# Kernel optimization log

Measured on AMD Instinct MI355X. Metric: run time of the kernel, lower is better.

Reference implementation:

```python
import jax, jax.numpy as jnp
import numpy as np

D_EQUI, D_INV, D_MSG, N_HEADS, D_FF = 64, 256, 64, 8, 256
D_EDGE_IN, D_EDGE_OUT = 64, 64
D_OUT = D_EQUI + N_HEADS + D_EDGE_OUT  # 136
IN_FEATS = 2 * D_MSG + D_EQUI + D_EDGE_IN  # 256
B, N = 4, 256
NEG_INF = -1e9  # finite stand-in for -inf in adj_to_attn_mask


def setup_inputs() -> dict:
    key = jax.random.key(0)
    ks = jax.random.split(key, 20)
    def rn(k, shape, scale):
        return jax.random.normal(k, shape, dtype=jnp.float32) * scale
    inp = {
        "equis": rn(ks[0], (B, N, 3, D_EQUI), 1.0),
        "invs": rn(ks[1], (B, N, D_INV), 1.0),
        "edges": rn(ks[2], (B, N, N, D_EDGE_IN), 1.0),
        "adj_matrix": jax.random.randint(ks[3], (B, N, N), 0, 2, dtype=jnp.int32),
        # _PairwiseMessages params
        "Wq": rn(ks[4], (D_MSG, D_INV), D_INV ** -0.5),
        "bq": jnp.zeros((D_MSG,), jnp.float32),
        "Wk": rn(ks[5], (D_MSG, D_INV), D_INV ** -0.5),
        "bk": jnp.zeros((D_MSG,), jnp.float32),
        "W1": rn(ks[6], (D_FF, IN_FEATS), IN_FEATS ** -0.5),
        "b1": jnp.zeros((D_FF,), jnp.float32),
        "W2": rn(ks[7], (D_OUT, D_FF), D_FF ** -0.5),
        "b2": jnp.zeros((D_OUT,), jnp.float32),
        # _EquiAttention params (no bias)
        "Wc": rn(ks[8], (D_EQUI, D_EQUI), D_EQUI ** -0.5),
        "Wa": rn(ks[9], (D_EQUI, D_EQUI), D_EQUI ** -0.5),
        # _InvAttention params
        "Wi": rn(ks[10], (D_INV, D_INV), D_INV ** -0.5),
        "bi": jnp.zeros((D_INV,), jnp.float32),
        "Wo": rn(ks[11], (D_INV, D_INV), D_INV ** -0.5),
        "bo": jnp.zeros((D_INV,), jnp.float32),
    }
    return inp


def _forward(equis, invs, edges, adj_matrix, Wq, bq, Wk, bk, W1, b1, W2, b2, Wc, Wa, Wi, bi, Wo, bo):
    # ---- _PairwiseMessages ----
    # per-channel dot products over the 3 coordinates: [B, Nq, Nk, d_equi]
    dotprods = jnp.einsum("bqcd,bkcd->bqkd", equis, equis)
    q_msg = invs @ Wq.T + bq          # [B, N, d_msg]
    k_msg = invs @ Wk.T + bk          # [B, N, d_msg]
    Nq = invs.shape[1]
    pairwise = jnp.concatenate(
        (
            jnp.broadcast_to(q_msg[:, :, None, :], (B, Nq, Nq, D_MSG)),
            jnp.broadcast_to(k_msg[:, None, :, :], (B, Nq, Nq, D_MSG)),
            dotprods,
            edges,
        ),
        axis=-1,
    )  # [B, Nq, Nk, in_feats]
    h = jax.nn.silu(pairwise @ W1.T + b1)
    messages = h @ W2.T + b2          # [B, Nq, Nk, d_out]

    equi_msg = messages[..., :D_EQUI]
    inv_msg = messages[..., D_EQUI : D_EQUI + N_HEADS]
    edge_out = messages[..., D_EQUI + N_HEADS :]

    attn_mask = jnp.where(adj_matrix > 0, 0.0, NEG_INF).astype(equi_msg.dtype)  # [B,Nq,Nk]

    # ---- _EquiAttention ----
    attn_e = jax.nn.softmax(equi_msg + attn_mask[..., None], axis=2)  # [B,Nq,Nk,d_equi]
    proj_equi = equis @ Wc.T                                          # [B,Nk,3,d_equi]
    attn_out_e = jnp.einsum("bqkd,bkcd->bqcd", attn_e, proj_equi)     # [B,Nq,3,d_equi]
    w_e = jnp.sqrt(jnp.sum(attn_e ** 2, axis=2))                      # [B,Nq,d_equi]
    attn_out_e = attn_out_e * w_e[:, :, None, :]
    equi_updates = attn_out_e @ Wa.T

    # ---- _InvAttention ----
    attn_i = jax.nn.softmax(inv_msg + attn_mask[..., None], axis=2)   # [B,Nq,Nk,H]
    proj_feats = invs @ Wi.T + bi                                     # [B,Nk,d_inv]
    head_feats = proj_feats.reshape(B, Nq, N_HEADS, D_INV // N_HEADS)
    attn_out_i = jnp.einsum("bqkh,bkhd->bqhd", attn_i, head_feats)    # [B,Nq,H,d_head]
    w_i = jnp.sqrt(jnp.sum(attn_i ** 2, axis=2))                      # [B,Nq,H]
    attn_out_i = attn_out_i * w_i[..., None]
    inv_updates = attn_out_i.reshape(B, Nq, D_INV) @ Wo.T + bo

    return equi_updates, inv_updates, edge_out


def reference(equis, invs, edges, adj_matrix, Wq, bq, Wk, bk, W1, b1, W2, b2, Wc, Wa, Wi, bi, Wo, bo):
    return _forward(equis, invs, edges, adj_matrix, Wq, bq, Wk, bk, W1, b1, W2, b2, Wc, Wa, Wi, bi, Wo, bo)
```

## Files before the change

kernel.cpp:

```cpp
#include <hip/hip_runtime.h>
#include <hip/hip_bf16.h>
#include <cstdint>


typedef __bf16 bf16x8_t __attribute__((ext_vector_type(8)));
typedef float  f32x4_t  __attribute__((ext_vector_type(4)));

#define SP 76
#define KV 32

__device__ __forceinline__ int swzX(int row, int col) {
    return row * 192 + (col ^ ((row & 7) << 3));
}
__device__ __forceinline__ int swzH(int row, int col) {
    return (row << 8) + (col ^ ((row & 7) << 3));
}

__device__ __forceinline__ bf16x8_t cvt8(f32x4_t a, f32x4_t b) {
    bf16x8_t r;
    r[0] = (__bf16)a.x; r[1] = (__bf16)a.y; r[2] = (__bf16)a.z; r[3] = (__bf16)a.w;
    r[4] = (__bf16)b.x; r[5] = (__bf16)b.y; r[6] = (__bf16)b.z; r[7] = (__bf16)b.w;
    return r;
}

__device__ __forceinline__ void lds_barrier() {
    asm volatile("s_waitcnt lgkmcnt(0)" ::: "memory");
    __builtin_amdgcn_s_barrier();
    asm volatile("" ::: "memory");
}

__global__ __launch_bounds__(256) void semla_pre(
    const float* __restrict__ invs, const float* __restrict__ equis,
    const float* __restrict__ Wq, const float* __restrict__ bq,
    const float* __restrict__ Wk, const float* __restrict__ bk,
    const float* __restrict__ Wc, const float* __restrict__ Wi, const float* __restrict__ bi,
    const float* __restrict__ W1, const float* __restrict__ W2,
    __bf16* __restrict__ W1bf, __bf16* __restrict__ W2bf,
    float* __restrict__ qc, float* __restrict__ kmsg,
    float* __restrict__ pTE, float* __restrict__ pTF)
{
    const int blk = blockIdx.x, tid = threadIdx.x;
    if (blk < 256) {
        const int r0 = blk * 4;
        __shared__ __align__(16) float sInv4[4][256];
        __shared__ __align__(16) float sEqu4[4][192];
        __shared__ __align__(16) float sQm4[4][64];
        #pragma unroll
        for (int j = 0; j < 4; ++j) {
            sInv4[j][tid] = invs[(size_t)(r0 + j) * 256 + tid];
            if (tid < 192) sEqu4[j][tid] = equis[(size_t)(r0 + j) * 192 + tid];
        }
        __syncthreads();
        {
            float acc[4] = {0.f, 0.f, 0.f, 0.f};
            const float* w = &Wi[tid * 256];
            for (int i = 0; i < 256; i += 4) {
                f32x4_t ww = *(const f32x4_t*)&w[i];
                #pragma unroll
                for (int j = 0; j < 4; ++j) {
                    const float* x = &sInv4[j][i];
                    acc[j] += ww.x * x[0] + ww.y * x[1] + ww.z * x[2] + ww.w * x[3];
                }
            }
            const float bb = bi[tid];
            #pragma unroll
            for (int j = 0; j < 4; ++j) {
                const int bb_ = (r0 + j) >> 8, nl = (r0 + j) & 255;
                pTF[((size_t)bb_ * 256 + tid) * 256 + nl] = acc[j] + bb;
            }
        }
        if (tid < 128) {
            const int d = tid & 63;
            const float* w = (tid < 64) ? &Wq[d * 256] : &Wk[d * 256];
            float acc[4] = {0.f, 0.f, 0.f, 0.f};
            for (int i = 0; i < 256; i += 4) {
                f32x4_t ww = *(const f32x4_t*)&w[i];
                #pragma unroll
                for (int j = 0; j < 4; ++j) {
                    const float* x = &sInv4[j][i];
                    acc[j] += ww.x * x[0] + ww.y * x[1] + ww.z * x[2] + ww.w * x[3];
                }
            }
            if (tid < 64) {
                const float bb = bq[d];
                #pragma unroll
                for (int j = 0; j < 4; ++j) sQm4[j][d] = acc[j] + bb;
            } else {
                const float bb = bk[d];
                #pragma unroll
                for (int j = 0; j < 4; ++j) kmsg[(size_t)(r0 + j) * 64 + d] = acc[j] + bb;
            }
        }
        if (tid < 192) {
            const int c = tid >> 6, e = tid & 63;
            const float* w = &Wc[e * 64];
            float acc[4] = {0.f, 0.f, 0.f, 0.f};
            for (int dd = 0; dd < 64; dd += 4) {
                f32x4_t ww = *(const f32x4_t*)&w[dd];
                #pragma unroll
                for (int j = 0; j < 4; ++j) {
                    const float* x = &sEqu4[j][c * 64 + dd];
                    acc[j] += ww.x * x[0] + ww.y * x[1] + ww.z * x[2] + ww.w * x[3];
                }
            }
            #pragma unroll
            for (int j = 0; j < 4; ++j) {
                const int bb_ = (r0 + j) >> 8, nl = (r0 + j) & 255;
                pTE[(((size_t)bb_ * 3 + c) * 64 + e) * 256 + nl] = acc[j];
            }
        }
        __syncthreads();
        {
            const float* w = &W1[tid * 256];
            float acc[4] = {0.f, 0.f, 0.f, 0.f};
            for (int d = 0; d < 64; d += 4) {
                f32x4_t ww = *(const f32x4_t*)&w[d];
                #pragma unroll
                for (int j = 0; j < 4; ++j) {
                    const float* x = &sQm4[j][d];
                    acc[j] += ww.x * x[0] + ww.y * x[1] + ww.z * x[2] + ww.w * x[3];
                }
            }
            #pragma unroll
            for (int j = 0; j < 4; ++j) qc[(size_t)(r0 + j) * 256 + tid] = acc[j];
        }
    } else if (blk < 268) {
        const int base = (blk - 256) * 4096;
        #pragma unroll
        for (int it = 0; it < 16; ++it) {
            const int e = base + it * 256 + tid;
            const int o = e / 192, k = e % 192;
            W1bf[e] = (__bf16)W1[o * 256 + 64 + k];
        }
    } else if (blk < 277) {
        const int base = (blk - 268) * 4096;
        #pragma unroll
        for (int it = 0; it < 16; ++it) {
            const int e = base + it * 256 + tid;
            const int o = e >> 8, cc = e & 255;
            const int src = (o < 64) ? (72 + o) : (o < 136 ? o - 64 : -1);
            W2bf[e] = (src >= 0) ? (__bf16)W2[src * 256 + cc] : (__bf16)0.f;
        }
    }
}

__global__ __launch_bounds__(512, 2) void semla_main(
    const float* __restrict__ equis, const float* __restrict__ edges,
    const int* __restrict__ adj,
    const __bf16* __restrict__ W1bf, const __bf16* __restrict__ W2bf,
    const float* __restrict__ qc, const float* __restrict__ kmsg,
    const float* __restrict__ pTE, const float* __restrict__ pTF,
    const float* __restrict__ b1, const float* __restrict__ b2,
    float* __restrict__ outE, float* __restrict__ outI, float* __restrict__ outEdge)
{
    const int bqid = ((blockIdx.x & 7) << 7) | (blockIdx.x >> 3);
    const int b = bqid >> 8;
    const int tid = threadIdx.x;
    const int wave = tid >> 6, lane = tid & 63;
    const int arow = lane & 15, kgrp = lane >> 4;

    __shared__ __align__(16) __bf16 sX[KV * 192];
    __shared__ __align__(16) __bf16 sH[KV * 256];
    __shared__ __align__(16) float  sS[KV * SP];
    __shared__ __align__(16) float  sB1[256];
    __shared__ __align__(16) float  sB2[144];
    __shared__ __align__(16) float  sEquiQ[192];
    __shared__ float sF[72], sL[72], sL2[72];
    __shared__ int   sAdj[KV];

    if (tid < 256) sB1[tid] = b1[tid] + qc[(size_t)bqid * 256 + tid];
    if (tid < 144) sB2[tid] = (tid < 64) ? b2[72 + tid] : (tid < 136 ? b2[tid - 64] : 0.f);
    if (tid < 192) sEquiQ[tid] = equis[(size_t)bqid * 192 + tid];

    bf16x8_t w1r[6][2];
    #pragma unroll
    for (int ks = 0; ks < 6; ++ks)
        #pragma unroll
        for (int cf = 0; cf < 2; ++cf)
            w1r[ks][cf] = *(const bf16x8_t*)
                &W1bf[((wave << 5) + (cf << 4) + arow) * 192 + ks * 32 + (kgrp << 3)];
    bf16x8_t w2r[8], w2r2[8];
    #pragma unroll
    for (int ks = 0; ks < 8; ++ks)
        w2r[ks] = *(const bf16x8_t*)
            &W2bf[(((wave << 4) + arow) << 8) + ks * 32 + (kgrp << 3)];
    if (wave == 7) {
        #pragma unroll
        for (int ks = 0; ks < 8; ++ks)
            w2r2[ks] = *(const bf16x8_t*)
                &W2bf[((128 + arow) << 8) + ks * 32 + (kgrp << 3)];
    }

    float m_run = -1e30f, l_run = 0.f, l2_run = 0.f;
    float m_rn2 = -1e30f, l_rn2 = 0.f, l2_rn2 = 0.f;
    float accE = 0.f;
    float accI = 0.f;
    const int c_e = tid >> 6, d_e = tid & 63;
    const int fidx = tid - 256, h_i = (tid - 256) >> 5;

    lds_barrier();

    for (int kt = 0; kt < 8; ++kt) {
        const int k0 = kt * KV;
        const int kb = b * 256 + k0;

        #pragma unroll
        for (int gi = 0; gi < 2; ++gi) {
            const int g = (gi == 0) ? tid : 512 + tid;
            if (gi == 1 && tid >= 256) continue;
            const int row = g / 24, c8 = (g % 24) << 3;
            if (c8 < 64) {
                const float* p = &kmsg[(size_t)(kb + row) * 64 + c8];
                *(bf16x8_t*)&sX[swzX(row, c8)] =
                    cvt8(*(const f32x4_t*)p, *(const f32x4_t*)(p + 4));
            } else if (c8 < 128) {
                const int d0 = c8 - 64;
                const float* ek = &equis[(size_t)(kb + row) * 192 + d0];
                f32x4_t e0a = *(const f32x4_t*)(ek),       e0b = *(const f32x4_t*)(ek + 4);
                f32x4_t e1a = *(const f32x4_t*)(ek + 64),  e1b = *(const f32x4_t*)(ek + 68);
                f32x4_t e2a = *(const f32x4_t*)(ek + 128), e2b = *(const f32x4_t*)(ek + 132);
                f32x4_t q0a = *(const f32x4_t*)&sEquiQ[d0],       q0b = *(const f32x4_t*)&sEquiQ[d0 + 4];
                f32x4_t q1a = *(const f32x4_t*)&sEquiQ[64 + d0],  q1b = *(const f32x4_t*)&sEquiQ[68 + d0];
                f32x4_t q2a = *(const f32x4_t*)&sEquiQ[128 + d0], q2b = *(const f32x4_t*)&sEquiQ[132 + d0];
                *(bf16x8_t*)&sX[swzX(row, c8)] =
                    cvt8(e0a * q0a + e1a * q1a + e2a * q2a,
                         e0b * q0b + e1b * q1b + e2b * q2b);
            } else {
                const float* p = &edges[((size_t)bqid * 256 + k0 + row) * 64 + (c8 - 128)];
                *(bf16x8_t*)&sX[swzX(row, c8)] =
                    cvt8(*(const f32x4_t*)p, *(const f32x4_t*)(p + 4));
            }
        }
        if (tid < KV) sAdj[tid] = adj[(size_t)bqid * 256 + k0 + tid];
        if (kt > 0) {
            const int k0P = k0 - KV;
            if (tid < 192) {
                float a = accE * sF[d_e];
                const float* pe = &pTE[(((size_t)b * 3 + c_e) * 64 + d_e) * 256 + k0P];
                #pragma unroll
                for (int t = 0; t < 8; ++t) {
                    f32x4_t w = *(const f32x4_t*)&pe[t * 4];
                    a += sS[(4 * t + 0) * SP + d_e] * w.x;
                    a += sS[(4 * t + 1) * SP + d_e] * w.y;
                    a += sS[(4 * t + 2) * SP + d_e] * w.z;
                    a += sS[(4 * t + 3) * SP + d_e] * w.w;
                }
                accE = a;
            }
            if (tid >= 256) {
                float a = accI * sF[64 + h_i];
                const float* pf = &pTF[((size_t)b * 256 + fidx) * 256 + k0P];
                #pragma unroll
                for (int t = 0; t < 8; ++t) {
                    f32x4_t w = *(const f32x4_t*)&pf[t * 4];
                    a += sS[(4 * t + 0) * SP + 64 + h_i] * w.x;
                    a += sS[(4 * t + 1) * SP + 64 + h_i] * w.y;
                    a += sS[(4 * t + 2) * SP + 64 + h_i] * w.z;
                    a += sS[(4 * t + 3) * SP + 64 + h_i] * w.w;
                }
                accI = a;
            }
        }
        lds_barrier();

        f32x4_t acc1[2][2];
        {
            const f32x4_t z = {0.f, 0.f, 0.f, 0.f};
            acc1[0][0] = z; acc1[0][1] = z; acc1[1][0] = z; acc1[1][1] = z;
        }
        __builtin_amdgcn_s_setprio(1);
        #pragma unroll
        for (int ks = 0; ks < 6; ++ks) {
            const int kk = ks * 32 + (kgrp << 3);
            bf16x8_t a0 = *(const bf16x8_t*)&sX[swzX(arow, kk)];
            bf16x8_t a1 = *(const bf16x8_t*)&sX[swzX(16 + arow, kk)];
            acc1[0][0] = __builtin_amdgcn_mfma_f32_16x16x32_bf16(a0, w1r[ks][0], acc1[0][0], 0, 0, 0);
            acc1[0][1] = __builtin_amdgcn_mfma_f32_16x16x32_bf16(a0, w1r[ks][1], acc1[0][1], 0, 0, 0);
            acc1[1][0] = __builtin_amdgcn_mfma_f32_16x16x32_bf16(a1, w1r[ks][0], acc1[1][0], 0, 0, 0);
            acc1[1][1] = __builtin_amdgcn_mfma_f32_16x16x32_bf16(a1, w1r[ks][1], acc1[1][1], 0, 0, 0);
        }
        __builtin_amdgcn_s_setprio(0);
        #pragma unroll
        for (int rt = 0; rt < 2; ++rt)
            #pragma unroll
            for (int cf = 0; cf < 2; ++cf) {
                const int ccol = (wave << 5) + (cf << 4) + arow;
                const float bb = sB1[ccol];
                #pragma unroll
                for (int j = 0; j < 4; ++j) {
                    const int row = (rt << 4) + (kgrp << 2) + j;
                    float x = acc1[rt][cf][j] + bb;
                    sH[swzH(row, ccol)] = (__bf16)(x / (1.f + __expf(-x)));
                }
            }
        lds_barrier();

        f32x4_t acc2[2], acc2b[2];
        {
            const f32x4_t z = {0.f, 0.f, 0.f, 0.f};
            acc2[0] = z; acc2[1] = z; acc2b[0] = z; acc2b[1] = z;
        }
        __builtin_amdgcn_s_setprio(1);
        #pragma unroll
        for (int ks = 0; ks < 8; ++ks) {
            const int kk = ks * 32 + (kgrp << 3);
            bf16x8_t a0 = *(const bf16x8_t*)&sH[swzH(arow, kk)];
            bf16x8_t a1 = *(const bf16x8_t*)&sH[swzH(16 + arow, kk)];
            acc2[0] = __builtin_amdgcn_mfma_f32_16x16x32_bf16(a0, w2r[ks], acc2[0], 0, 0, 0);
            acc2[1] = __builtin_amdgcn_mfma_f32_16x16x32_bf16(a1, w2r[ks], acc2[1], 0, 0, 0);
            if (wave == 7) {
                acc2b[0] = __builtin_amdgcn_mfma_f32_16x16x32_bf16(a0, w2r2[ks], acc2b[0], 0, 0, 0);
                acc2b[1] = __builtin_amdgcn_mfma_f32_16x16x32_bf16(a1, w2r2[ks], acc2b[1], 0, 0, 0);
            }
        }
        __builtin_amdgcn_s_setprio(0);
        const int col = (wave << 4) + arow;
        if (wave < 4) {
            const float bb2 = sB2[col];
            #pragma unroll
            for (int rt = 0; rt < 2; ++rt)
                #pragma unroll
                for (int j = 0; j < 4; ++j) {
                    const int r = (rt << 4) + (kgrp << 2) + j;
                    outEdge[((size_t)bqid * 256 + k0 + r) * 64 + col] = acc2[rt][j] + bb2;
                }
        } else {
            const int ch = col - 64;
            const float bb2 = sB2[col];
            float s_[8]; int ad_[8];
            float xm = -1e30f;
            #pragma unroll
            for (int rt = 0; rt < 2; ++rt)
                #pragma unroll
                for (int j = 0; j < 4; ++j) {
                    const int r = (rt << 4) + (kgrp << 2) + j;
                    const float v = acc2[rt][j] + bb2;
                    s_[rt * 4 + j] = v;
                    ad_[rt * 4 + j] = sAdj[r];
                    if (ad_[rt * 4 + j]) xm = fmaxf(xm, v);
                }
            xm = fmaxf(xm, __shfl_xor(xm, 16));
            xm = fmaxf(xm, __shfl_xor(xm, 32));
            const float mN = fmaxf(m_run, xm);
            const float f = __expf(m_run - mN);
            float s1 = 0.f, s2 = 0.f;
            #pragma unroll
            for (int rt = 0; rt < 2; ++rt)
                #pragma unroll
                for (int j = 0; j < 4; ++j) {
                    const int r = (rt << 4) + (kgrp << 2) + j;
                    const float p = ad_[rt * 4 + j] ? __expf(s_[rt * 4 + j] - mN) : 0.f;
                    sS[r * SP + ch] = p;
                    s1 += p; s2 += p * p;
                }
            s1 += __shfl_xor(s1, 16); s1 += __shfl_xor(s1, 32);
            s2 += __shfl_xor(s2, 16); s2 += __shfl_xor(s2, 32);
            l_run = l_run * f + s1;
            l2_run = l2_run * f * f + s2;
            m_run = mN;
            if (kgrp == 0) sF[ch] = f;
        }
        if (wave == 7) {
            const float bb3 = sB2[128 + (arow & 7)];
            float s_[8]; int ad_[8];
            float xm = -1e30f;
            #pragma unroll
            for (int rt = 0; rt < 2; ++rt)
                #pragma unroll
                for (int j = 0; j < 4; ++j) {
                    const int r = (rt << 4) + (kgrp << 2) + j;
                    const float v = acc2b[rt][j] + bb3;
                    s_[rt * 4 + j] = v;
                    ad_[rt * 4 + j] = sAdj[r];
                    if (ad_[rt * 4 + j]) xm = fmaxf(xm, v);
                }
            xm = fmaxf(xm, __shfl_xor(xm, 16));
            xm = fmaxf(xm, __shfl_xor(xm, 32));
            const float mN = fmaxf(m_rn2, xm);
            const float f = __expf(m_rn2 - mN);
            float s1 = 0.f, s2 = 0.f;
            #pragma unroll
            for (int rt = 0; rt < 2; ++rt)
                #pragma unroll
                for (int j = 0; j < 4; ++j) {
                    const int r = (rt << 4) + (kgrp << 2) + j;
                    const float p = ad_[rt * 4 + j] ? __expf(s_[rt * 4 + j] - mN) : 0.f;
                    if (arow < 8) sS[r * SP + 64 + arow] = p;
                    s1 += p; s2 += p * p;
                }
            s1 += __shfl_xor(s1, 16); s1 += __shfl_xor(s1, 32);
            s2 += __shfl_xor(s2, 16); s2 += __shfl_xor(s2, 32);
            l_rn2 = l_rn2 * f + s1;
            l2_rn2 = l2_rn2 * f * f + s2;
            m_rn2 = mN;
            if (kgrp == 0 && arow < 8) sF[64 + arow] = f;
        }
        lds_barrier();
    }

    {
        const int k0P = 224;
        if (tid < 192) {
            float a = accE * sF[d_e];
            const float* pe = &pTE[(((size_t)b * 3 + c_e) * 64 + d_e) * 256 + k0P];
            #pragma unroll
            for (int t = 0; t < 8; ++t) {
                f32x4_t w = *(const f32x4_t*)&pe[t * 4];
                a += sS[(4 * t + 0) * SP + d_e] * w.x;
                a += sS[(4 * t + 1) * SP + d_e] * w.y;
                a += sS[(4 * t + 2) * SP + d_e] * w.z;
                a += sS[(4 * t + 3) * SP + d_e] * w.w;
            }
            accE = a;
        }
        if (tid >= 256) {
            float a = accI * sF[64 + h_i];
            const float* pf = &pTF[((size_t)b * 256 + fidx) * 256 + k0P];
            #pragma unroll
            for (int t = 0; t < 8; ++t) {
                f32x4_t w = *(const f32x4_t*)&pf[t * 4];
                a += sS[(4 * t + 0) * SP + 64 + h_i] * w.x;
                a += sS[(4 * t + 1) * SP + 64 + h_i] * w.y;
                a += sS[(4 * t + 2) * SP + 64 + h_i] * w.z;
                a += sS[(4 * t + 3) * SP + 64 + h_i] * w.w;
            }
            accI = a;
        }
    }

    if (wave >= 4 && kgrp == 0) {
        const int ch = ((wave - 4) << 4) + arow;
        sL[ch] = l_run; sL2[ch] = l2_run;
        if (wave == 7 && arow < 8) { sL[64 + arow] = l_rn2; sL2[64 + arow] = l2_rn2; }
    }
    lds_barrier();
    if (tid < 192) {
        const float ll = sL[d_e];
        outE[(size_t)bqid * 192 + tid] = accE * sqrtf(sL2[d_e]) / (ll * ll);
    }
    if (tid >= 256) {
        const float ll = sL[64 + h_i];
        outI[(size_t)bqid * 256 + fidx] = accI * sqrtf(sL2[64 + h_i]) / (ll * ll);
    }
}

__global__ __launch_bounds__(256) void semla_post(
    const float* __restrict__ Wa, const float* __restrict__ Wo,
    const float* __restrict__ bo,
    float* __restrict__ outE, float* __restrict__ outI)
{
    __shared__ __align__(16) float hE[4][192];
    __shared__ __align__(16) float hI[4][256];
    const int blk = blockIdx.x, tid = threadIdx.x;
    const int r0 = blk * 4;
    #pragma unroll
    for (int r = 0; r < 4; ++r) {
        if (tid < 192) hE[r][tid] = outE[(size_t)(r0 + r) * 192 + tid];
        hI[r][tid] = outI[(size_t)(r0 + r) * 256 + tid];
    }
    __syncthreads();
    if (tid < 192) {
        const int c = tid >> 6, e = tid & 63;
        float wa[64];
        #pragma unroll
        for (int d = 0; d < 64; d += 4) {
            f32x4_t w = *(const f32x4_t*)&Wa[e * 64 + d];
            wa[d] = w.x; wa[d + 1] = w.y; wa[d + 2] = w.z; wa[d + 3] = w.w;
        }
        #pragma unroll
        for (int r = 0; r < 4; ++r) {
            float s = 0.f;
            #pragma unroll
            for (int d = 0; d < 64; ++d) s += hE[r][c * 64 + d] * wa[d];
            outE[((size_t)(r0 + r) * 3 + c) * 64 + e] = s;
        }
    }
    {
        const float bb = bo[tid];
        const float* wo = &Wo[tid * 256];
        #pragma unroll
        for (int r = 0; r < 4; ++r) {
            float s = 0.f;
            for (int i = 0; i < 256; i += 4) {
                f32x4_t w = *(const f32x4_t*)&wo[i];
                s += w.x * hI[r][i] + w.y * hI[r][i + 1]
                   + w.z * hI[r][i + 2] + w.w * hI[r][i + 3];
            }
            outI[(size_t)(r0 + r) * 256 + tid] = s + bb;
        }
    }
}

extern "C" void kernel_launch(void* const* d_in, const int* in_sizes, int n_in,
                              void* d_out, int out_size, void* d_ws, size_t ws_size,
                              hipStream_t stream) {
    (void)in_sizes; (void)n_in; (void)out_size; (void)ws_size;
    const float* equis = (const float*)d_in[0];
    const float* invs  = (const float*)d_in[1];
    const float* edges = (const float*)d_in[2];
    const int*   adj   = (const int*)d_in[3];
    const float* Wq = (const float*)d_in[4];
    const float* bq = (const float*)d_in[5];
    const float* Wk = (const float*)d_in[6];
    const float* bk = (const float*)d_in[7];
    const float* W1 = (const float*)d_in[8];
    const float* b1 = (const float*)d_in[9];
    const float* W2 = (const float*)d_in[10];
    const float* b2 = (const float*)d_in[11];
    const float* Wc = (const float*)d_in[12];
    const float* Wa = (const float*)d_in[13];
    const float* Wi = (const float*)d_in[14];
    const float* bi = (const float*)d_in[15];
    const float* Wo = (const float*)d_in[16];
    const float* bo = (const float*)d_in[17];

    float* out = (float*)d_out;
    float* outE    = out;
    float* outI    = out + 196608;
    float* outEdge = out + 458752;

    char* ws = (char*)d_ws;
    __bf16* W1bf = (__bf16*)(ws);
    __bf16* W2bf = (__bf16*)(ws + 98304);
    float* qc    = (float*)(ws + 172032);
    float* kmsg  = (float*)(ws + 1220608);
    float* pTE   = (float*)(ws + 1482752);
    float* pTF   = (float*)(ws + 2269184);

    semla_pre<<<277, 256, 0, stream>>>(invs, equis, Wq, bq, Wk, bk, Wc, Wi, bi,
                                       W1, W2, W1bf, W2bf, qc, kmsg, pTE, pTF);
    semla_main<<<1024, 512, 0, stream>>>(equis, edges, adj, W1bf, W2bf, qc, kmsg,
                                         pTE, pTF, b1, b2,
                                         outE, outI, outEdge);
    semla_post<<<256, 256, 0, stream>>>(Wa, Wo, bo, outE, outI);
}
```

Measured before the change: 297.7 us.

## Double key tile to 64 and stream W2 tail rows from global

Raises the key-tile size from 32 to 64, so the fused MLP/softmax loop runs 4 iterations instead of 8. Each wave now handles 4 row tiles per MFMA pass, reusing the register-resident W1/W2 fragments over more rows and halving barriers and online-softmax rescale steps. To limit register pressure, wave 7's extra W2 rows are loaded from global memory inside the k-loop rather than held in registers, and the adjacency flags are packed into a bitmask. The tradeoffs are higher VGPR and LDS use, which may lower occupancy, plus repeated global loads of W2 for wave 7.

```diff
diff --git a/kernel.cpp b/kernel.cpp
--- a/kernel.cpp
+++ b/kernel.cpp
@@ -7,7 +7,7 @@
 typedef float  f32x4_t  __attribute__((ext_vector_type(4)));
 
 #define SP 76
-#define KV 32
+#define KV 64
 
 __device__ __forceinline__ int swzX(int row, int col) {
     return row * 192 + (col ^ ((row & 7) << 3));
@@ -179,17 +179,11 @@
         for (int cf = 0; cf < 2; ++cf)
             w1r[ks][cf] = *(const bf16x8_t*)
                 &W1bf[((wave << 5) + (cf << 4) + arow) * 192 + ks * 32 + (kgrp << 3)];
-    bf16x8_t w2r[8], w2r2[8];
+    bf16x8_t w2r[8];
     #pragma unroll
     for (int ks = 0; ks < 8; ++ks)
         w2r[ks] = *(const bf16x8_t*)
             &W2bf[(((wave << 4) + arow) << 8) + ks * 32 + (kgrp << 3)];
-    if (wave == 7) {
-        #pragma unroll
-        for (int ks = 0; ks < 8; ++ks)
-            w2r2[ks] = *(const bf16x8_t*)
-                &W2bf[((128 + arow) << 8) + ks * 32 + (kgrp << 3)];
-    }
 
     float m_run = -1e30f, l_run = 0.f, l2_run = 0.f;
     float m_rn2 = -1e30f, l_rn2 = 0.f, l2_rn2 = 0.f;
@@ -200,14 +194,13 @@
 
     lds_barrier();
 
-    for (int kt = 0; kt < 8; ++kt) {
+    for (int kt = 0; kt < 4; ++kt) {
         const int k0 = kt * KV;
         const int kb = b * 256 + k0;
 
         #pragma unroll
-        for (int gi = 0; gi < 2; ++gi) {
-            const int g = (gi == 0) ? tid : 512 + tid;
-            if (gi == 1 && tid >= 256) continue;
+        for (int it = 0; it < 3; ++it) {
+            const int g = it * 512 + tid;
             const int row = g / 24, c8 = (g % 24) << 3;
             if (c8 < 64) {
                 const float* p = &kmsg[(size_t)(kb + row) * 64 + c8];
@@ -238,7 +231,7 @@
                 float a = accE * sF[d_e];
                 const float* pe = &pTE[(((size_t)b * 3 + c_e) * 64 + d_e) * 256 + k0P];
                 #pragma unroll
-                for (int t = 0; t < 8; ++t) {
+                for (int t = 0; t < 16; ++t) {
                     f32x4_t w = *(const f32x4_t*)&pe[t * 4];
                     a += sS[(4 * t + 0) * SP + d_e] * w.x;
                     a += sS[(4 * t + 1) * SP + d_e] * w.y;
@@ -251,7 +244,7 @@
                 float a = accI * sF[64 + h_i];
                 const float* pf = &pTF[((size_t)b * 256 + fidx) * 256 + k0P];
                 #pragma unroll
-                for (int t = 0; t < 8; ++t) {
+                for (int t = 0; t < 16; ++t) {
                     f32x4_t w = *(const f32x4_t*)&pf[t * 4];
                     a += sS[(4 * t + 0) * SP + 64 + h_i] * w.x;
                     a += sS[(4 * t + 1) * SP + 64 + h_i] * w.y;
@@ -263,25 +256,29 @@
         }
         lds_barrier();
 
-        f32x4_t acc1[2][2];
+        f32x4_t acc1[4][2];
         {
             const f32x4_t z = {0.f, 0.f, 0.f, 0.f};
-            acc1[0][0] = z; acc1[0][1] = z; acc1[1][0] = z; acc1[1][1] = z;
+            #pragma unroll
+            for (int rt = 0; rt < 4; ++rt) { acc1[rt][0] = z; acc1[rt][1] = z; }
         }
         __builtin_amdgcn_s_setprio(1);
         #pragma unroll
         for (int ks = 0; ks < 6; ++ks) {
             const int kk = ks * 32 + (kgrp << 3);
-            bf16x8_t a0 = *(const bf16x8_t*)&sX[swzX(arow, kk)];
-            bf16x8_t a1 = *(const bf16x8_t*)&sX[swzX(16 + arow, kk)];
-            acc1[0][0] = __builtin_amdgcn_mfma_f32_16x16x32_bf16(a0, w1r[ks][0], acc1[0][0], 0, 0, 0);
-            acc1[0][1] = __builtin_amdgcn_mfma_f32_16x16x32_bf16(a0, w1r[ks][1], acc1[0][1], 0, 0, 0);
-            acc1[1][0] = __builtin_amdgcn_mfma_f32_16x16x32_bf16(a1, w1r[ks][0], acc1[1][0], 0, 0, 0);
-            acc1[1][1] = __builtin_amdgcn_mfma_f32_16x16x32_bf16(a1, w1r[ks][1], acc1[1][1], 0, 0, 0);
+            bf16x8_t a[4];
+            #pragma unroll
+            for (int rt = 0; rt < 4; ++rt)
+                a[rt] = *(const bf16x8_t*)&sX[swzX((rt << 4) + arow, kk)];
+            #pragma unroll
+            for (int rt = 0; rt < 4; ++rt) {
+                acc1[rt][0] = __builtin_amdgcn_mfma_f32_16x16x32_bf16(a[rt], w1r[ks][0], acc1[rt][0], 0, 0, 0);
+                acc1[rt][1] = __builtin_amdgcn_mfma_f32_16x16x32_bf16(a[rt], w1r[ks][1], acc1[rt][1], 0, 0, 0);
+            }
         }
         __builtin_amdgcn_s_setprio(0);
         #pragma unroll
-        for (int rt = 0; rt < 2; ++rt)
+        for (int rt = 0; rt < 4; ++rt)
             #pragma unroll
             for (int cf = 0; cf < 2; ++cf) {
                 const int ccol = (wave << 5) + (cf << 4) + arow;
@@ -295,22 +292,28 @@
             }
         lds_barrier();
 
-        f32x4_t acc2[2], acc2b[2];
+        f32x4_t acc2[4], acc2b[4];
         {
             const f32x4_t z = {0.f, 0.f, 0.f, 0.f};
-            acc2[0] = z; acc2[1] = z; acc2b[0] = z; acc2b[1] = z;
+            #pragma unroll
+            for (int rt = 0; rt < 4; ++rt) { acc2[rt] = z; acc2b[rt] = z; }
         }
         __builtin_amdgcn_s_setprio(1);
         #pragma unroll
         for (int ks = 0; ks < 8; ++ks) {
             const int kk = ks * 32 + (kgrp << 3);
-            bf16x8_t a0 = *(const bf16x8_t*)&sH[swzH(arow, kk)];
-            bf16x8_t a1 = *(const bf16x8_t*)&sH[swzH(16 + arow, kk)];
-            acc2[0] = __builtin_amdgcn_mfma_f32_16x16x32_bf16(a0, w2r[ks], acc2[0], 0, 0, 0);
-            acc2[1] = __builtin_amdgcn_mfma_f32_16x16x32_bf16(a1, w2r[ks], acc2[1], 0, 0, 0);
+            bf16x8_t a[4];
+            #pragma unroll
+            for (int rt = 0; rt < 4; ++rt)
+                a[rt] = *(const bf16x8_t*)&sH[swzH((rt << 4) + arow, kk)];
+            #pragma unroll
+            for (int rt = 0; rt < 4; ++rt)
+                acc2[rt] = __builtin_amdgcn_mfma_f32_16x16x32_bf16(a[rt], w2r[ks], acc2[rt], 0, 0, 0);
             if (wave == 7) {
-                acc2b[0] = __builtin_amdgcn_mfma_f32_16x16x32_bf16(a0, w2r2[ks], acc2b[0], 0, 0, 0);
-                acc2b[1] = __builtin_amdgcn_mfma_f32_16x16x32_bf16(a1, w2r2[ks], acc2b[1], 0, 0, 0);
+                bf16x8_t bw = *(const bf16x8_t*)&W2bf[((128 + arow) << 8) + kk];
+                #pragma unroll
+                for (int rt = 0; rt < 4; ++rt)
+                    acc2b[rt] = __builtin_amdgcn_mfma_f32_16x16x32_bf16(a[rt], bw, acc2b[rt], 0, 0, 0);
             }
         }
         __builtin_amdgcn_s_setprio(0);
@@ -318,7 +321,7 @@
         if (wave < 4) {
             const float bb2 = sB2[col];
             #pragma unroll
-            for (int rt = 0; rt < 2; ++rt)
+            for (int rt = 0; rt < 4; ++rt)
                 #pragma unroll
                 for (int j = 0; j < 4; ++j) {
                     const int r = (rt << 4) + (kgrp << 2) + j;
@@ -327,17 +330,17 @@
         } else {
             const int ch = col - 64;
             const float bb2 = sB2[col];
-            float s_[8]; int ad_[8];
+            float s_[16];
+            unsigned adm = 0;
             float xm = -1e30f;
             #pragma unroll
-            for (int rt = 0; rt < 2; ++rt)
+            for (int rt = 0; rt < 4; ++rt)
                 #pragma unroll
                 for (int j = 0; j < 4; ++j) {
                     const int r = (rt << 4) + (kgrp << 2) + j;
                     const float v = acc2[rt][j] + bb2;
                     s_[rt * 4 + j] = v;
-                    ad_[rt * 4 + j] = sAdj[r];
-                    if (ad_[rt * 4 + j]) xm = fmaxf(xm, v);
+                    if (sAdj[r]) { adm |= (1u << (rt * 4 + j)); xm = fmaxf(xm, v); }
                 }
             xm = fmaxf(xm, __shfl_xor(xm, 16));
             xm = fmaxf(xm, __shfl_xor(xm, 32));
@@ -345,11 +348,12 @@
             const float f = __expf(m_run - mN);
             float s1 = 0.f, s2 = 0.f;
             #pragma unroll
-            for (int rt = 0; rt < 2; ++rt)
+            for (int rt = 0; rt < 4; ++rt)
                 #pragma unroll
                 for (int j = 0; j < 4; ++j) {
                     const int r = (rt << 4) + (kgrp << 2) + j;
-                    const float p = ad_[rt * 4 + j] ? __expf(s_[rt * 4 + j] - mN) : 0.f;
+                    const float p = ((adm >> (rt * 4 + j)) & 1u)
+                                    ? __expf(s_[rt * 4 + j] - mN) : 0.f;
                     sS[r * SP + ch] = p;
                     s1 += p; s2 += p * p;
                 }
@@ -362,17 +366,17 @@
         }
         if (wave == 7) {
             const float bb3 = sB2[128 + (arow & 7)];
-            float s_[8]; int ad_[8];
+            float s_[16];
+            unsigned adm = 0;
             float xm = -1e30f;
             #pragma unroll
-            for (int rt = 0; rt < 2; ++rt)
+            for (int rt = 0; rt < 4; ++rt)
                 #pragma unroll
                 for (int j = 0; j < 4; ++j) {
                     const int r = (rt << 4) + (kgrp << 2) + j;
                     const float v = acc2b[rt][j] + bb3;
                     s_[rt * 4 + j] = v;
-                    ad_[rt * 4 + j] = sAdj[r];
-                    if (ad_[rt * 4 + j]) xm = fmaxf(xm, v);
+                    if (sAdj[r]) { adm |= (1u << (rt * 4 + j)); xm = fmaxf(xm, v); }
                 }
             xm = fmaxf(xm, __shfl_xor(xm, 16));
             xm = fmaxf(xm, __shfl_xor(xm, 32));
@@ -380,11 +384,12 @@
             const float f = __expf(m_rn2 - mN);
             float s1 = 0.f, s2 = 0.f;
             #pragma unroll
-            for (int rt = 0; rt < 2; ++rt)
+            for (int rt = 0; rt < 4; ++rt)
                 #pragma unroll
                 for (int j = 0; j < 4; ++j) {
                     const int r = (rt << 4) + (kgrp << 2) + j;
-                    const float p = ad_[rt * 4 + j] ? __expf(s_[rt * 4 + j] - mN) : 0.f;
+                    const float p = ((adm >> (rt * 4 + j)) & 1u)
+                                    ? __expf(s_[rt * 4 + j] - mN) : 0.f;
                     if (arow < 8) sS[r * SP + 64 + arow] = p;
                     s1 += p; s2 += p * p;
                 }
@@ -399,12 +404,12 @@
     }
 
     {
-        const int k0P = 224;
+        const int k0P = 192;
         if (tid < 192) {
             float a = accE * sF[d_e];
             const float* pe = &pTE[(((size_t)b * 3 + c_e) * 64 + d_e) * 256 + k0P];
             #pragma unroll
-            for (int t = 0; t < 8; ++t) {
+            for (int t = 0; t < 16; ++t) {
                 f32x4_t w = *(const f32x4_t*)&pe[t * 4];
                 a += sS[(4 * t + 0) * SP + d_e] * w.x;
                 a += sS[(4 * t + 1) * SP + d_e] * w.y;
@@ -417,7 +422,7 @@
             float a = accI * sF[64 + h_i];
             const float* pf = &pTF[((size_t)b * 256 + fidx) * 256 + k0P];
             #pragma unroll
-            for (int t = 0; t < 8; ++t) {
+            for (int t = 0; t < 16; ++t) {
                 f32x4_t w = *(const f32x4_t*)&pf[t * 4];
                 a += sS[(4 * t + 0) * SP + 64 + h_i] * w.x;
                 a += sS[(4 * t + 1) * SP + 64 + h_i] * w.y;
```

After: 332.4 us. 11.6% more time.
